# Performance work log

Measured on AMD Instinct MI355X. Metric: run time of the kernel, lower is better.

Reference implementation:

```python
import jax, jax.numpy as jnp
import numpy as np
import math

# ---- hyperparameters (init_kwargs) ----
D = 2              # spatial dimension
MTOT = 65          # quadrature nodes per dimension (odd)
LENGTHSCALE = 0.1  # SE kernel lengthscale
OUTPUTSCALE = 1.0  # SE kernel variance
SIGMASQ = 0.05     # observation noise variance
CG_ITERS = 30      # fixed CG iteration count (replaces tol-based early stopping)
N_TRAIN = 100000
N_TEST = 50000
TWO_PI = 2.0 * math.pi


def setup_inputs() -> dict:
    key = jax.random.key(0)
    k1, k2, k3 = jax.random.split(key, 3)
    x = jax.random.uniform(k1, (N_TRAIN, D), dtype=jnp.float32)
    y = jax.random.normal(k2, (N_TRAIN,), dtype=jnp.float32)
    x_new = jax.random.uniform(k3, (N_TEST, D), dtype=jnp.float32)
    return {"x": x, "y": y, "x_new": x_new}


def _phases(col, h, freqs, isign):
    # exp(isign * i * 2*pi*h * x * k), shape [N, K]
    return jnp.exp((1j * isign * TWO_PI) * (h * col[:, None] * freqs[None, :]).astype(jnp.float32))


def _nudft_type1(pts, c, h, freqs):
    # fk[a,b] = sum_n c_n exp(-2*pi*i*h*(k_a x_n0 + k_b x_n1)); separable tensor grid
    E0 = _phases(pts[:, 0], h, freqs, -1.0)
    E1 = _phases(pts[:, 1], h, freqs, -1.0)
    return jnp.einsum('n,na,nb->ab', c.astype(jnp.complex64), E0, E1)


def _nudft_type2(pts, fk, h, freqs):
    # f_n = sum_{a,b} fk[a,b] exp(+2*pi*i*h*(k_a x_n0 + k_b x_n1))
    E0 = _phases(pts[:, 0], h, freqs, +1.0)
    E1 = _phases(pts[:, 1], h, freqs, +1.0)
    return jnp.einsum('ab,na,nb->n', fk, E0, E1)


def _cg(A, b, iters):
    # complex Hermitian-PSD conjugate gradients, fixed iteration count
    x0 = jnp.zeros_like(b)
    r0 = b
    rs0 = jnp.real(jnp.vdot(r0, r0))

    def step(carry, _):
        xk, r, p, rs = carry
        Ap = A(p)
        alpha = rs / jnp.real(jnp.vdot(p, Ap))
        xk = xk + alpha * p
        r = r - alpha * Ap
        rs_new = jnp.real(jnp.vdot(r, r))
        p = r + (rs_new / rs) * p
        return (xk, r, p, rs_new), None

    (xk, _, _, _), _ = jax.lax.scan(step, (x0, r0, r0, rs0), None, length=iters)
    return xk


def _forward(x, y, x_new):
    m = (MTOT - 1) // 2
    # geometry / quadrature (get_xis): domain extent L, spacing h = 1/L, grid k = -m..m
    x_all = jnp.concatenate((x, x_new), axis=0)
    L = jnp.max(jnp.max(x_all, axis=0) - jnp.min(x_all, axis=0))
    L = jnp.where(L <= 1e-9, jnp.float32(1.0), L)
    h = (1.0 / L).astype(jnp.float32)
    k = (jnp.arange(MTOT) - m).astype(jnp.float32)
    xis_1d = h * k
    X0, X1 = jnp.meshgrid(xis_1d, xis_1d, indexing='ij')
    sq = X0 * X0 + X1 * X1  # [MTOT, MTOT] squared frequency norm
    # squared-exponential spectral density S(s) = sigma_f^2 (2*pi*l^2)^(d/2) exp(-2*pi^2*l^2 |s|^2)
    l2 = LENGTHSCALE * LENGTHSCALE
    spec = OUTPUTSCALE * (TWO_PI * l2) ** (D / 2) * jnp.exp((-2.0 * math.pi ** 2 * l2) * sq)
    ws = jnp.sqrt(spec * h ** D).reshape(-1).astype(jnp.complex64)  # [M]

    # rhs = ws * F^H y  (type-1 NUFFT, exact NUDFT)
    rhs = ws * _nudft_type1(x, y, h, k).reshape(-1)

    # Toeplitz convolution vector v[o] = sum_n exp(-2*pi*i*h*o.x_n), offsets -(mtot-1)..(mtot-1)
    kk = (jnp.arange(2 * MTOT - 1) - (MTOT - 1)).astype(jnp.float32)
    Ev0 = _phases(x[:, 0], h, kk, -1.0)
    Ev1 = _phases(x[:, 1], h, kk, -1.0)
    v = jnp.einsum('na,nb->ab', Ev0, Ev1)  # [2M-1, 2M-1]
    # circularly align offset 0 to index 0, precompute FFT
    v_circ = jnp.roll(v, shift=(-(MTOT - 1), -(MTOT - 1)), axis=(0, 1))
    vhat = jnp.fft.fftn(v_circ)
    s_fft = (2 * MTOT - 1, 2 * MTOT - 1)

    def toeplitz_apply(w):  # w: [MTOT, MTOT] complex
        W = jnp.fft.fftn(w, s=s_fft)
        full = jnp.fft.ifftn(vhat * W)
        return full[:MTOT, :MTOT]

    def A_mean(beta):  # (W F^H F W + sigma^2 I) beta, beta flat [M]
        wb = (ws * beta).reshape(MTOT, MTOT)
        Tw = toeplitz_apply(wb).reshape(-1)
        return ws * Tw + SIGMASQ * beta

    beta = _cg(A_mean, rhs, CG_ITERS)
    # posterior mean at test points via type-2 NUFFT
    yhat = jnp.real(_nudft_type2(x_new, (ws * beta).reshape(MTOT, MTOT), h, k))
    return yhat


def reference(x, y, x_new):
    return _forward(x, y, x_new)
```

## Files before the change

kernel.cpp:

```cpp
#include <hip/hip_runtime.h>
#include <math.h>

#define M2 4225
#define NTRAIN 100000
#define NTEST 50000
#define CGITERS 30
#define TWO_PI_D 6.283185307179586476925287
#define TPI32 6.28318530717958647692f

#define F_H 0
#define F_RS 1
#define F_PAP 2
#define F_RSN 3
#define F_WS 8
#define F_RHS 4234
#define F_X 12684
#define F_R 21134
#define F_P 29584
#define F_AP 38034
#define F_PB 46484
#define F_VF 50710
#define F_VHAT 83992
#define F_PROD 117274
#define D_VPART 125330
#define D_FKPART 2271890

#define NCHUNK 128
#define PTSB2 782
#define VHALF 8385
#define VH2 16770
#define FKHALF 2145
#define FH2 4290

__device__ __forceinline__ unsigned fkey(float f){
  unsigned u = __float_as_uint(f);
  return (u & 0x80000000u) ? ~u : (u | 0x80000000u);
}
__device__ __forceinline__ float fdec(unsigned k){
  unsigned u = (k & 0x80000000u) ? (k & 0x7fffffffu) : ~k;
  return __uint_as_float(u);
}

__global__ void k_init(unsigned* mm){
  if (threadIdx.x == 0){
    mm[0] = 0xFFFFFFFFu; mm[1] = 0u; mm[2] = 0xFFFFFFFFu; mm[3] = 0u;
  }
}

__global__ void k_minmax(const float* __restrict__ x, const float* __restrict__ xn,
                         unsigned* __restrict__ mm){
  int tid = blockIdx.x * blockDim.x + threadIdx.x;
  int str = gridDim.x * blockDim.x;
  float mn0 = 1e30f, mx0 = -1e30f, mn1 = 1e30f, mx1 = -1e30f;
  const float2* a = (const float2*)x;
  for (int i = tid; i < NTRAIN; i += str){
    float2 v = a[i];
    mn0 = fminf(mn0, v.x); mx0 = fmaxf(mx0, v.x);
    mn1 = fminf(mn1, v.y); mx1 = fmaxf(mx1, v.y);
  }
  const float2* b = (const float2*)xn;
  for (int i = tid; i < NTEST; i += str){
    float2 v = b[i];
    mn0 = fminf(mn0, v.x); mx0 = fmaxf(mx0, v.x);
    mn1 = fminf(mn1, v.y); mx1 = fmaxf(mx1, v.y);
  }
  for (int off = 32; off; off >>= 1){
    mn0 = fminf(mn0, __shfl_xor(mn0, off, 64));
    mx0 = fmaxf(mx0, __shfl_xor(mx0, off, 64));
    mn1 = fminf(mn1, __shfl_xor(mn1, off, 64));
    mx1 = fmaxf(mx1, __shfl_xor(mx1, off, 64));
  }
  if ((threadIdx.x & 63) == 0){
    atomicMin(&mm[0], fkey(mn0)); atomicMax(&mm[1], fkey(mx0));
    atomicMin(&mm[2], fkey(mn1)); atomicMax(&mm[3], fkey(mx1));
  }
}

__global__ void k_setup(float* __restrict__ wsf){
  const unsigned* mm = (const unsigned*)(wsf + 4);
  float mn0 = fdec(mm[0]), mx0 = fdec(mm[1]);
  float mn1 = fdec(mm[2]), mx1 = fdec(mm[3]);
  float d0 = __fsub_rn(mx0, mn0), d1 = __fsub_rn(mx1, mn1);
  float L = fmaxf(d0, d1);
  if (L <= 1e-9f) L = 1.0f;
  float hf = __fdiv_rn(1.0f, L);
  if (threadIdx.x == 0) wsf[F_H] = hf;
  const float c0f = (float)(TWO_PI_D * 0.01);
  const float c1f = (float)(-2.0 * 9.869604401089358618834 * 0.01);
  float h2f = __fmul_rn(hf, hf);
  for (int e = threadIdx.x; e < M2; e += blockDim.x){
    int r = e / 65, c = e - r * 65;
    float xi0 = __fmul_rn(hf, (float)(r - 32));
    float xi1 = __fmul_rn(hf, (float)(c - 32));
    float sq = __fadd_rn(__fmul_rn(xi0, xi0), __fmul_rn(xi1, xi1));
    float spec = __fmul_rn(c0f, expf(__fmul_rn(c1f, sq)));
    wsf[F_WS + e] = sqrtf(__fmul_rn(spec, h2f));
  }
}

__launch_bounds__(256)
__global__ void k_vfk(const float* __restrict__ x, const float* __restrict__ y,
                      const float* __restrict__ wsf,
                      double* __restrict__ vpart, double* __restrict__ fkpart){
  __shared__ double2 aL[16][80];
  __shared__ double2 bL[16][32];
  __shared__ float hxs[16][2];
  __shared__ float ys[16];
  const float hf = wsf[F_H];
  const int tid = threadIdx.x;
  const int t0 = tid >> 4, t1 = tid & 15;
  const bool isV = (blockIdx.y < 5);
  const int colbase = (isV ? blockIdx.y : (blockIdx.y - 5)) * 32;
  const int p0 = blockIdx.x * PTSB2;
  const int pend = min(p0 + PTSB2, NTRAIN);

  if (isV){
    double2 acc[5][2];
    #pragma unroll
    for (int k = 0; k < 5; ++k){ acc[k][0] = make_double2(0.0, 0.0); acc[k][1] = make_double2(0.0, 0.0); }
    for (int base = p0; base < pend; base += 16){
      if (tid < 32){
        int p = tid >> 1, d = tid & 1;
        int gp = base + p;
        hxs[p][d] = (gp < pend) ? __fmul_rn(hf, x[2 * gp + d]) : 0.f;
      }
      __syncthreads();
      for (int i = tid; i < 16 * 80; i += 256){
        int p = i / 80;
        int o = i - p * 80;
        int gp = base + p;
        double2 va = make_double2(0.0, 0.0);
        if (gp < pend && o < 65){
          float t = __fmul_rn(hxs[p][0], (float)o);
          float sn, cs; sincosf(__fmul_rn(TPI32, t), &sn, &cs);
          va = make_double2((double)cs, (double)(-sn));
        }
        aL[p][o] = va;
      }
      for (int i = tid; i < 16 * 32; i += 256){
        int p = i >> 5, c = i & 31;
        int gp = base + p;
        int j = colbase + c;
        double2 vb = make_double2(0.0, 0.0);
        if (gp < pend && j < 129){
          float t = __fmul_rn(hxs[p][1], (float)(j - 64));
          float sn, cs; sincosf(__fmul_rn(TPI32, t), &sn, &cs);
          vb = make_double2((double)cs, (double)(-sn));
        }
        bL[p][c] = vb;
      }
      __syncthreads();
      #pragma unroll 1
      for (int p = 0; p < 16; ++p){
        double2 bv0 = bL[p][t1];
        double2 bv1 = bL[p][t1 + 16];
        double2 av[5];
        #pragma unroll
        for (int k = 0; k < 5; ++k) av[k] = aL[p][t0 + 16 * k];
        #pragma unroll
        for (int k = 0; k < 5; ++k){
          acc[k][0].x += av[k].x * bv0.x - av[k].y * bv0.y;
          acc[k][0].y += av[k].x * bv0.y + av[k].y * bv0.x;
          acc[k][1].x += av[k].x * bv1.x - av[k].y * bv1.y;
          acc[k][1].y += av[k].x * bv1.y + av[k].y * bv1.x;
        }
      }
      __syncthreads();
    }
    double* outp = vpart + (size_t)blockIdx.x * VH2;
    #pragma unroll
    for (int k = 0; k < 5; ++k){
      int o0 = t0 + 16 * k;
      if (o0 < 65){
        #pragma unroll
        for (int cc = 0; cc < 2; ++cc){
          int jcol = colbase + t1 + 16 * cc;
          if (jcol < 129){
            int e = o0 * 129 + jcol;
            outp[2 * e] = acc[k][cc].x;
            outp[2 * e + 1] = acc[k][cc].y;
          }
        }
      }
    }
  } else {
    double2 acc[3][2];
    #pragma unroll
    for (int k = 0; k < 3; ++k){ acc[k][0] = make_double2(0.0, 0.0); acc[k][1] = make_double2(0.0, 0.0); }
    for (int base = p0; base < pend; base += 16){
      if (tid < 32){
        int p = tid >> 1, d = tid & 1;
        int gp = base + p;
        hxs[p][d] = (gp < pend) ? __fmul_rn(hf, x[2 * gp + d]) : 0.f;
      } else if (tid < 48){
        int p = tid - 32;
        int gp = base + p;
        ys[p] = (gp < pend) ? y[gp] : 0.f;
      }
      __syncthreads();
      for (int i = tid; i < 16 * 48; i += 256){
        int p = i / 48, o = i - p * 48;
        int gp = base + p;
        double2 val = make_double2(0.0, 0.0);
        if (o < 33 && gp < pend){
          float t = __fmul_rn(hxs[p][0], (float)o);
          float sn, cs; sincosf(__fmul_rn(TPI32, t), &sn, &cs);
          val = make_double2((double)__fmul_rn(ys[p], cs), (double)__fmul_rn(ys[p], -sn));
        }
        aL[p][o] = val;
      }
      for (int i = tid; i < 16 * 32; i += 256){
        int p = i >> 5, c = i & 31;
        int gp = base + p;
        int j = colbase + c;
        double2 vb = make_double2(0.0, 0.0);
        if (gp < pend && j < 65){
          float t = __fmul_rn(hxs[p][1], (float)(j - 32));
          float sn, cs; sincosf(__fmul_rn(TPI32, t), &sn, &cs);
          vb = make_double2((double)cs, (double)(-sn));
        }
        bL[p][c] = vb;
      }
      __syncthreads();
      #pragma unroll 1
      for (int p = 0; p < 16; ++p){
        double2 bv0 = bL[p][t1];
        double2 bv1 = bL[p][t1 + 16];
        double2 av[3];
        #pragma unroll
        for (int k = 0; k < 3; ++k) av[k] = aL[p][t0 + 16 * k];
        #pragma unroll
        for (int k = 0; k < 3; ++k){
          acc[k][0].x += av[k].x * bv0.x - av[k].y * bv0.y;
          acc[k][0].y += av[k].x * bv0.y + av[k].y * bv0.x;
          acc[k][1].x += av[k].x * bv1.x - av[k].y * bv1.y;
          acc[k][1].y += av[k].x * bv1.y + av[k].y * bv1.x;
        }
      }
      __syncthreads();
    }
    double* outp = fkpart + (size_t)blockIdx.x * FH2;
    #pragma unroll
    for (int k = 0; k < 3; ++k){
      int o0 = t0 + 16 * k;
      if (o0 < 33){
        #pragma unroll
        for (int cc = 0; cc < 2; ++cc){
          int jcol = colbase + t1 + 16 * cc;
          if (jcol < 65){
            int e = o0 * 65 + jcol;
            outp[2 * e] = acc[k][cc].x;
            outp[2 * e + 1] = acc[k][cc].y;
          }
        }
      }
    }
  }
}

__global__ void k_reduce_v(const double* __restrict__ wsd, float* __restrict__ wsf){
  int e = blockIdx.x * blockDim.x + threadIdx.x;
  if (e >= VHALF) return;
  const double* vp = wsd + D_VPART;
  double sr = 0.0, si = 0.0;
  for (int k = 0; k < NCHUNK; ++k){
    sr += vp[(size_t)k * VH2 + 2 * e];
    si += vp[(size_t)k * VH2 + 2 * e + 1];
  }
  float r32 = (float)sr, i32 = (float)si;
  int o0 = e / 129, j = e - o0 * 129;
  float2* vF = (float2*)(wsf + F_VF);
  vF[(o0 + 64) * 129 + j] = make_float2(r32, i32);
  if (o0 > 0) vF[(64 - o0) * 129 + (128 - j)] = make_float2(r32, -i32);
}

__global__ void k_reduce_fk(const double* __restrict__ wsd, float* __restrict__ wsf){
  int e = blockIdx.x * blockDim.x + threadIdx.x;
  if (e >= FKHALF) return;
  const double* fp = wsd + D_FKPART;
  double sr = 0.0, si = 0.0;
  for (int k = 0; k < NCHUNK; ++k){
    sr += fp[(size_t)k * FH2 + 2 * e];
    si += fp[(size_t)k * FH2 + 2 * e + 1];
  }
  float fr = (float)sr, fi = (float)si;
  int a = e / 65, c = e - a * 65;
  int ef = (a + 32) * 65 + c;
  float wf = wsf[F_WS + ef];
  float* rhs = wsf + F_RHS;
  rhs[2 * ef] = __fmul_rn(wf, fr);
  rhs[2 * ef + 1] = __fmul_rn(wf, fi);
  if (a > 0){
    int ef2 = (32 - a) * 65 + (64 - c);
    float wf2 = wsf[F_WS + ef2];
    rhs[2 * ef2] = __fmul_rn(wf2, fr);
    rhs[2 * ef2 + 1] = -__fmul_rn(wf2, fi);
  }
}

__launch_bounds__(192)
__global__ void k_vhat(float* __restrict__ wsf){
  __shared__ double twc[129], tws[129];
  __shared__ double t1r[129], t1i[129];
  int p = blockIdx.x, t = threadIdx.x;
  if (t < 129){
    double ang = TWO_PI_D * (double)t / 129.0;
    double s, c; sincos(ang, &s, &c);
    twc[t] = c; tws[t] = s;
  }
  __syncthreads();
  if (t < 129){
    const float2* vF = (const float2*)(wsf + F_VF);
    int n = t;
    int nsrc = (n + 64) % 129;
    double ar = 0.0, ai = 0.0;
    for (int m = 0; m < 129; ++m){
      float2 v = vF[((m + 64) % 129) * 129 + nsrc];
      int idx = (p * m) % 129;
      double wr = twc[idx], wi = -tws[idx];
      ar += (double)v.x * wr - (double)v.y * wi;
      ai += (double)v.x * wi + (double)v.y * wr;
    }
    t1r[n] = ar; t1i[n] = ai;
  }
  __syncthreads();
  if (t < 129){
    int q = t;
    double ar = 0.0, ai = 0.0;
    for (int n = 0; n < 129; ++n){
      int idx = (q * n) % 129;
      double wr = twc[idx], wi = -tws[idx];
      ar += t1r[n] * wr - t1i[n] * wi;
      ai += t1r[n] * wi + t1i[n] * wr;
    }
    ((float2*)(wsf + F_VHAT))[p * 129 + q] = make_float2((float)ar, (float)ai);
  }
}

__global__ void k_cg_init(float* __restrict__ wsf){
  int e = blockIdx.x * blockDim.x + threadIdx.x;
  if (e >= M2) return;
  const float2* rhs = (const float2*)(wsf + F_RHS);
  float2 b = rhs[e];
  ((float2*)(wsf + F_X))[e] = make_float2(0.f, 0.f);
  ((float2*)(wsf + F_R))[e] = b;
  ((float2*)(wsf + F_P))[e] = b;
  wsf[F_PB + e] = __fadd_rn(__fmul_rn(b.x, b.x), __fmul_rn(b.y, b.y));
}

__device__ __forceinline__ float pw_leaf(const float* d, int o, int n){
  float r0 = d[o], r1 = d[o+1], r2 = d[o+2], r3 = d[o+3];
  float r4 = d[o+4], r5 = d[o+5], r6 = d[o+6], r7 = d[o+7];
  int i = 8;
  int lim = n - (n & 7);
  for (; i < lim; i += 8){
    r0 = __fadd_rn(r0, d[o+i]);   r1 = __fadd_rn(r1, d[o+i+1]);
    r2 = __fadd_rn(r2, d[o+i+2]); r3 = __fadd_rn(r3, d[o+i+3]);
    r4 = __fadd_rn(r4, d[o+i+4]); r5 = __fadd_rn(r5, d[o+i+5]);
    r6 = __fadd_rn(r6, d[o+i+6]); r7 = __fadd_rn(r7, d[o+i+7]);
  }
  float res = __fadd_rn(__fadd_rn(__fadd_rn(r0, r1), __fadd_rn(r2, r3)),
                        __fadd_rn(__fadd_rn(r4, r5), __fadd_rn(r6, r7)));
  for (; i < n; ++i) res = __fadd_rn(res, d[o+i]);
  return res;
}

__device__ __forceinline__ void pw_tree(const float* pb, float* T, int tid){
  if (tid < 16){
    const int tb[16] = {0,264,528,792,1056,1320,1584,1848,
                        2112,2376,2640,2904,3168,3432,3696,3960};
    int base = tb[tid];
    int sz3 = (tid == 15) ? 73 : 72;
    float L0 = pw_leaf(pb, base, 128);
    float L1 = pw_leaf(pb, base + 128, 64);
    float L2 = pw_leaf(pb, base + 192, sz3);
    T[tid] = __fadd_rn(L0, __fadd_rn(L1, L2));
  }
  __syncthreads();
  if (tid == 0){
    float s0 = __fadd_rn(__fadd_rn(T[0], T[1]), __fadd_rn(T[2], T[3]));
    float s1 = __fadd_rn(__fadd_rn(T[4], T[5]), __fadd_rn(T[6], T[7]));
    float s2 = __fadd_rn(__fadd_rn(T[8], T[9]), __fadd_rn(T[10], T[11]));
    float s3 = __fadd_rn(__fadd_rn(T[12], T[13]), __fadd_rn(T[14], T[15]));
    T[0] = __fadd_rn(__fadd_rn(s0, s1), __fadd_rn(s2, s3));
  }
}

__launch_bounds__(256)
__global__ void k_pair0(float* __restrict__ wsf){
  __shared__ float pb[M2];
  __shared__ float T[16];
  int tid = threadIdx.x;
  for (int i = tid; i < M2; i += 256) pb[i] = wsf[F_PB + i];
  __syncthreads();
  pw_tree(pb, T, tid);
  __syncthreads();
  if (tid == 0) wsf[F_RS] = T[0];
}

__launch_bounds__(192)
__global__ void k_wfft(float* __restrict__ wsf){
  __shared__ double twc[129], tws[129];
  __shared__ double t1r[65], t1i[65];
  int pr = blockIdx.x, t = threadIdx.x;
  if (t < 129){
    double ang = TWO_PI_D * (double)t / 129.0;
    double s, c; sincos(ang, &s, &c);
    twc[t] = c; tws[t] = s;
  }
  __syncthreads();
  if (t < 65){
    const float2* P = (const float2*)(wsf + F_P);
    const float* W = wsf + F_WS;
    int n = t;
    double ar = 0.0, ai = 0.0;
    for (int m = 0; m < 65; ++m){
      int e = m * 65 + n;
      float2 p = P[e];
      float w = W[e];
      float wbr = __fmul_rn(w, p.x), wbi = __fmul_rn(w, p.y);
      int idx = (pr * m) % 129;
      double wr = twc[idx], wi = -tws[idx];
      ar += (double)wbr * wr - (double)wbi * wi;
      ai += (double)wbr * wi + (double)wbi * wr;
    }
    t1r[n] = ar; t1i[n] = ai;
  }
  __syncthreads();
  if (t < 129){
    int q = t;
    double ar = 0.0, ai = 0.0;
    for (int n = 0; n < 65; ++n){
      int idx = (q * n) % 129;
      double wr = twc[idx], wi = -tws[idx];
      ar += t1r[n] * wr - t1i[n] * wi;
      ai += t1r[n] * wi + t1i[n] * wr;
    }
    float Wr = (float)ar, Wi = (float)ai;
    float2 v = ((const float2*)(wsf + F_VHAT))[pr * 129 + q];
    float prre = __fsub_rn(__fmul_rn(v.x, Wr), __fmul_rn(v.y, Wi));
    float prim = __fadd_rn(__fmul_rn(v.x, Wi), __fmul_rn(v.y, Wr));
    ((float2*)(wsf + F_PROD))[pr * 129 + q] = make_float2(prre, prim);
  }
}

__launch_bounds__(192)
__global__ void k_ifft(float* __restrict__ wsf){
  __shared__ double twc[129], tws[129];
  __shared__ double ur[129], ui[129];
  int m = blockIdx.x, t = threadIdx.x;
  if (t < 129){
    double ang = TWO_PI_D * (double)t / 129.0;
    double s, c; sincos(ang, &s, &c);
    twc[t] = c; tws[t] = s;
  }
  __syncthreads();
  if (t < 129){
    const float2* prod = (const float2*)(wsf + F_PROD);
    int q = t;
    double ar = 0.0, ai = 0.0;
    for (int pr = 0; pr < 129; ++pr){
      float2 v = prod[pr * 129 + q];
      int idx = (m * pr) % 129;
      double wr = twc[idx], wi = tws[idx];
      ar += (double)v.x * wr - (double)v.y * wi;
      ai += (double)v.x * wi + (double)v.y * wr;
    }
    const double sc = 1.0 / 129.0;
    ur[q] = ar * sc; ui[q] = ai * sc;
  }
  __syncthreads();
  if (t < 65){
    int n = t;
    double ar = 0.0, ai = 0.0;
    for (int q = 0; q < 129; ++q){
      int idx = (n * q) % 129;
      double wr = twc[idx], wi = tws[idx];
      ar += ur[q] * wr - ui[q] * wi;
      ai += ur[q] * wi + ui[q] * wr;
    }
    const double sc = 1.0 / 129.0;
    float Twr = (float)(ar * sc), Twi = (float)(ai * sc);
    int e = m * 65 + n;
    float w = wsf[F_WS + e];
    float2 p = ((const float2*)(wsf + F_P))[e];
    float Apx = __fadd_rn(__fmul_rn(w, Twr), __fmul_rn(0.05f, p.x));
    float Apy = __fadd_rn(__fmul_rn(w, Twi), __fmul_rn(0.05f, p.y));
    ((float2*)(wsf + F_AP))[e] = make_float2(Apx, Apy);
    wsf[F_PB + e] = __fadd_rn(__fmul_rn(p.x, Apx), __fmul_rn(p.y, Apy));
  }
}

__launch_bounds__(256)
__global__ void k_cgstep(float* __restrict__ wsf){
  __shared__ float pb[M2];
  __shared__ float T[16];
  __shared__ float sh[2];
  int tid = threadIdx.x;
  for (int i = tid; i < M2; i += 256) pb[i] = wsf[F_PB + i];
  __syncthreads();
  pw_tree(pb, T, tid);
  __syncthreads();
  if (tid == 0){
    float rs = wsf[F_RS];
    sh[1] = rs;
    sh[0] = __fdiv_rn(rs, T[0]);
  }
  __syncthreads();
  float alpha = sh[0];
  float2* X = (float2*)(wsf + F_X);
  float2* R = (float2*)(wsf + F_R);
  float2* P = (float2*)(wsf + F_P);
  const float2* AP = (const float2*)(wsf + F_AP);
  for (int e = tid; e < M2; e += 256){
    float2 p = P[e], ap = AP[e], xv = X[e], rv = R[e];
    xv.x = __fadd_rn(xv.x, __fmul_rn(alpha, p.x));
    xv.y = __fadd_rn(xv.y, __fmul_rn(alpha, p.y));
    rv.x = __fsub_rn(rv.x, __fmul_rn(alpha, ap.x));
    rv.y = __fsub_rn(rv.y, __fmul_rn(alpha, ap.y));
    X[e] = xv; R[e] = rv;
    pb[e] = __fadd_rn(__fmul_rn(rv.x, rv.x), __fmul_rn(rv.y, rv.y));
  }
  __syncthreads();
  pw_tree(pb, T, tid);
  __syncthreads();
  if (tid == 0){
    float rsn = T[0];
    sh[0] = __fdiv_rn(rsn, sh[1]);
    wsf[F_RS] = rsn;
  }
  __syncthreads();
  float beta = sh[0];
  for (int e = tid; e < M2; e += 256){
    float2 rv = R[e], p = P[e];
    P[e] = make_float2(__fadd_rn(rv.x, __fmul_rn(beta, p.x)),
                       __fadd_rn(rv.y, __fmul_rn(beta, p.y)));
  }
}

__launch_bounds__(256)
__global__ void k_predict(const float* __restrict__ xn, const float* __restrict__ wsf,
                          float* __restrict__ out){
  __shared__ double fbRe[M2];
  __shared__ double fbIm[M2];
  const float hf = wsf[F_H];
  const float* wsq = wsf + F_WS;
  const float2* xb = (const float2*)(wsf + F_X);
  int tid = threadIdx.x;
  for (int i = tid; i < M2; i += 256){
    float w = wsq[i]; float2 q = xb[i];
    fbRe[i] = (double)__fmul_rn(w, q.x);
    fbIm[i] = (double)__fmul_rn(w, q.y);
  }
  __syncthreads();
  int lane = tid & 63;
  int wid = (blockIdx.x * 256 + tid) >> 6;
  int nw = (gridDim.x * 256) >> 6;
  for (int n = wid; n < NTEST; n += nw){
    float hx0 = __fmul_rn(hf, xn[2 * n]);
    float hx1 = __fmul_rn(hf, xn[2 * n + 1]);
    float t0 = __fmul_rn(hx0, (float)(lane - 32));
    float s0, c0; sincosf(__fmul_rn(TPI32, t0), &s0, &c0);
    float t1 = __fmul_rn(hx1, (float)(lane - 32));
    float s1, c1; sincosf(__fmul_rn(TPI32, t1), &s1, &c1);
    float t0x = __fmul_rn(hx0, 32.0f);
    float s0x, c0x; sincosf(__fmul_rn(TPI32, t0x), &s0x, &c0x);
    float t1x = __fmul_rn(hx1, 32.0f);
    float s1x, c1x; sincosf(__fmul_rn(TPI32, t1x), &s1x, &c1x);
    double e0r = (double)c0, e0i = (double)s0;
    double e1r = (double)c1, e1i = (double)s1;
    double gr = 0.0, gi = 0.0;
    for (int a = 0; a < 64; ++a){
      double er = __shfl(e0r, a, 64);
      double ei = __shfl(e0i, a, 64);
      double fr = fbRe[a * 65 + lane];
      double fi = fbIm[a * 65 + lane];
      gr += fr * er - fi * ei;
      gi += fr * ei + fi * er;
    }
    {
      double fr = fbRe[64 * 65 + lane], fi = fbIm[64 * 65 + lane];
      gr += fr * (double)c0x - fi * (double)s0x;
      gi += fr * (double)s0x + fi * (double)c0x;
    }
    double contrib = gr * e1r - gi * e1i;
    {
      double fr = fbRe[lane * 65 + 64], fi = fbIm[lane * 65 + 64];
      double ur = fr * e0r - fi * e0i;
      double ui = fr * e0i + fi * e0r;
      contrib += ur * (double)c1x - ui * (double)s1x;
      if (lane == 0){
        double fr2 = fbRe[64 * 65 + 64], fi2 = fbIm[64 * 65 + 64];
        double vr = fr2 * (double)c0x - fi2 * (double)s0x;
        double vi = fr2 * (double)s0x + fi2 * (double)c0x;
        contrib += vr * (double)c1x - vi * (double)s1x;
      }
    }
    for (int off = 32; off; off >>= 1) contrib += __shfl_xor(contrib, off, 64);
    if (lane == 0) out[n] = (float)contrib;
  }
}

extern "C" void kernel_launch(void* const* d_in, const int* in_sizes, int n_in,
                              void* d_out, int out_size, void* d_ws, size_t ws_size,
                              hipStream_t stream){
  const float* x = (const float*)d_in[0];
  const float* y = (const float*)d_in[1];
  const float* xnew = (const float*)d_in[2];
  float* wsf = (float*)d_ws;
  double* wsd = (double*)d_ws;
  float* out = (float*)d_out;
  unsigned* mm = (unsigned*)(wsf + 4);

  k_init<<<1, 64, 0, stream>>>(mm);
  k_minmax<<<256, 256, 0, stream>>>(x, xnew, mm);
  k_setup<<<1, 256, 0, stream>>>(wsf);
  k_vfk<<<dim3(NCHUNK, 8), 256, 0, stream>>>(x, y, wsf, wsd + D_VPART, wsd + D_FKPART);
  k_reduce_v<<<33, 256, 0, stream>>>(wsd, wsf);
  k_reduce_fk<<<9, 256, 0, stream>>>(wsd, wsf);
  k_vhat<<<129, 192, 0, stream>>>(wsf);
  k_cg_init<<<17, 256, 0, stream>>>(wsf);
  k_pair0<<<1, 256, 0, stream>>>(wsf);
  for (int it = 0; it < CGITERS; ++it){
    k_wfft<<<129, 192, 0, stream>>>(wsf);
    k_ifft<<<65, 192, 0, stream>>>(wsf);
    k_cgstep<<<1, 256, 0, stream>>>(wsf);
  }
  k_predict<<<256, 256, 0, stream>>>(xnew, wsf, out);
}
```

Before: 2.173 ms.

## Fuse CG iteration loop into one persistent kernel with grid barriers

Replaces the 90 per-iteration launches (forward DFT, inverse DFT, CG update) with a single persistent kernel of 129 blocks that synchronises through a two-level atomic grid barrier kept in workspace memory. It also replaces the modulo twiddle index computation with an incremental add-and-wrap. The aim is to remove kernel launch and drain overhead across the 30 iterations. In exchange, all 129 blocks must be co-resident for the barrier to avoid deadlock, and blocks sit idle during the single-block CG update phase.

```diff
diff --git a/kernel.cpp b/kernel.cpp
--- a/kernel.cpp
+++ b/kernel.cpp
@@ -22,6 +22,7 @@
 #define F_VF 50710
 #define F_VHAT 83992
 #define F_PROD 117274
+#define U_BAR 150592
 #define D_VPART 125330
 #define D_FKPART 2271890
 
@@ -31,6 +32,7 @@
 #define VH2 16770
 #define FKHALF 2145
 #define FH2 4290
+#define NBLK 129
 
 __device__ __forceinline__ unsigned fkey(float f){
   unsigned u = __float_as_uint(f);
@@ -339,6 +341,7 @@
 
 __global__ void k_cg_init(float* __restrict__ wsf){
   int e = blockIdx.x * blockDim.x + threadIdx.x;
+  if (e < 320) ((unsigned*)wsf)[U_BAR + e] = 0u;
   if (e >= M2) return;
   const float2* rhs = (const float2*)(wsf + F_RHS);
   float2 b = rhs[e];
@@ -398,143 +401,176 @@
   if (tid == 0) wsf[F_RS] = T[0];
 }
 
-__launch_bounds__(192)
-__global__ void k_wfft(float* __restrict__ wsf){
+__device__ __forceinline__ void gridbar(unsigned* bar){
+  __syncthreads();
+  if (threadIdx.x == 0){
+    unsigned* cnt = bar + (blockIdx.x >> 3) * 16;
+    unsigned* top = bar + 272;
+    unsigned* gen = bar + 288;
+    int gsize = ((blockIdx.x >> 3) < 16) ? 8 : 1;
+    __threadfence();
+    unsigned g = __hip_atomic_load(gen, __ATOMIC_RELAXED, __HIP_MEMORY_SCOPE_AGENT);
+    unsigned old = __hip_atomic_fetch_add(cnt, 1u, __ATOMIC_RELAXED, __HIP_MEMORY_SCOPE_AGENT);
+    if ((int)old == gsize - 1){
+      __hip_atomic_store(cnt, 0u, __ATOMIC_RELAXED, __HIP_MEMORY_SCOPE_AGENT);
+      unsigned oldt = __hip_atomic_fetch_add(top, 1u, __ATOMIC_ACQ_REL, __HIP_MEMORY_SCOPE_AGENT);
+      if (oldt == 16u){
+        __hip_atomic_store(top, 0u, __ATOMIC_RELAXED, __HIP_MEMORY_SCOPE_AGENT);
+        __hip_atomic_fetch_add(gen, 1u, __ATOMIC_RELEASE, __HIP_MEMORY_SCOPE_AGENT);
+      } else {
+        while (__hip_atomic_load(gen, __ATOMIC_RELAXED, __HIP_MEMORY_SCOPE_AGENT) == g){
+          __builtin_amdgcn_s_sleep(2);
+        }
+      }
+    } else {
+      while (__hip_atomic_load(gen, __ATOMIC_RELAXED, __HIP_MEMORY_SCOPE_AGENT) == g){
+        __builtin_amdgcn_s_sleep(2);
+      }
+    }
+    __threadfence();
+  }
+  __syncthreads();
+}
+
+__launch_bounds__(256)
+__global__ void k_cgloop(float* __restrict__ wsf){
   __shared__ double twc[129], tws[129];
-  __shared__ double t1r[65], t1i[65];
-  int pr = blockIdx.x, t = threadIdx.x;
+  __shared__ double d1[129], d2[129];
+  __shared__ float pb[M2];
+  __shared__ float T[16];
+  __shared__ float sh[2];
+  const int bid = blockIdx.x;
+  const int t = threadIdx.x;
+  unsigned* bar = ((unsigned*)wsf) + U_BAR;
   if (t < 129){
     double ang = TWO_PI_D * (double)t / 129.0;
     double s, c; sincos(ang, &s, &c);
     twc[t] = c; tws[t] = s;
   }
   __syncthreads();
-  if (t < 65){
-    const float2* P = (const float2*)(wsf + F_P);
-    const float* W = wsf + F_WS;
-    int n = t;
-    double ar = 0.0, ai = 0.0;
-    for (int m = 0; m < 65; ++m){
-      int e = m * 65 + n;
-      float2 p = P[e];
-      float w = W[e];
-      float wbr = __fmul_rn(w, p.x), wbi = __fmul_rn(w, p.y);
-      int idx = (pr * m) % 129;
-      double wr = twc[idx], wi = -tws[idx];
-      ar += (double)wbr * wr - (double)wbi * wi;
-      ai += (double)wbr * wi + (double)wbi * wr;
-    }
-    t1r[n] = ar; t1i[n] = ai;
-  }
-  __syncthreads();
-  if (t < 129){
-    int q = t;
-    double ar = 0.0, ai = 0.0;
-    for (int n = 0; n < 65; ++n){
-      int idx = (q * n) % 129;
-      double wr = twc[idx], wi = -tws[idx];
-      ar += t1r[n] * wr - t1i[n] * wi;
-      ai += t1r[n] * wi + t1i[n] * wr;
-    }
-    float Wr = (float)ar, Wi = (float)ai;
-    float2 v = ((const float2*)(wsf + F_VHAT))[pr * 129 + q];
-    float prre = __fsub_rn(__fmul_rn(v.x, Wr), __fmul_rn(v.y, Wi));
-    float prim = __fadd_rn(__fmul_rn(v.x, Wi), __fmul_rn(v.y, Wr));
-    ((float2*)(wsf + F_PROD))[pr * 129 + q] = make_float2(prre, prim);
-  }
-}
-
-__launch_bounds__(192)
-__global__ void k_ifft(float* __restrict__ wsf){
-  __shared__ double twc[129], tws[129];
-  __shared__ double ur[129], ui[129];
-  int m = blockIdx.x, t = threadIdx.x;
-  if (t < 129){
-    double ang = TWO_PI_D * (double)t / 129.0;
-    double s, c; sincos(ang, &s, &c);
-    twc[t] = c; tws[t] = s;
-  }
-  __syncthreads();
-  if (t < 129){
-    const float2* prod = (const float2*)(wsf + F_PROD);
-    int q = t;
-    double ar = 0.0, ai = 0.0;
-    for (int pr = 0; pr < 129; ++pr){
-      float2 v = prod[pr * 129 + q];
-      int idx = (m * pr) % 129;
-      double wr = twc[idx], wi = tws[idx];
-      ar += (double)v.x * wr - (double)v.y * wi;
-      ai += (double)v.x * wi + (double)v.y * wr;
-    }
-    const double sc = 1.0 / 129.0;
-    ur[q] = ar * sc; ui[q] = ai * sc;
-  }
-  __syncthreads();
-  if (t < 65){
-    int n = t;
-    double ar = 0.0, ai = 0.0;
-    for (int q = 0; q < 129; ++q){
-      int idx = (n * q) % 129;
-      double wr = twc[idx], wi = tws[idx];
-      ar += ur[q] * wr - ui[q] * wi;
-      ai += ur[q] * wi + ui[q] * wr;
-    }
-    const double sc = 1.0 / 129.0;
-    float Twr = (float)(ar * sc), Twi = (float)(ai * sc);
-    int e = m * 65 + n;
-    float w = wsf[F_WS + e];
-    float2 p = ((const float2*)(wsf + F_P))[e];
-    float Apx = __fadd_rn(__fmul_rn(w, Twr), __fmul_rn(0.05f, p.x));
-    float Apy = __fadd_rn(__fmul_rn(w, Twi), __fmul_rn(0.05f, p.y));
-    ((float2*)(wsf + F_AP))[e] = make_float2(Apx, Apy);
-    wsf[F_PB + e] = __fadd_rn(__fmul_rn(p.x, Apx), __fmul_rn(p.y, Apy));
-  }
-}
-
-__launch_bounds__(256)
-__global__ void k_cgstep(float* __restrict__ wsf){
-  __shared__ float pb[M2];
-  __shared__ float T[16];
-  __shared__ float sh[2];
-  int tid = threadIdx.x;
-  for (int i = tid; i < M2; i += 256) pb[i] = wsf[F_PB + i];
-  __syncthreads();
-  pw_tree(pb, T, tid);
-  __syncthreads();
-  if (tid == 0){
-    float rs = wsf[F_RS];
-    sh[1] = rs;
-    sh[0] = __fdiv_rn(rs, T[0]);
-  }
-  __syncthreads();
-  float alpha = sh[0];
+  float2* PROD = (float2*)(wsf + F_PROD);
+  const float2* VHAT = (const float2*)(wsf + F_VHAT);
   float2* X = (float2*)(wsf + F_X);
   float2* R = (float2*)(wsf + F_R);
   float2* P = (float2*)(wsf + F_P);
-  const float2* AP = (const float2*)(wsf + F_AP);
-  for (int e = tid; e < M2; e += 256){
-    float2 p = P[e], ap = AP[e], xv = X[e], rv = R[e];
-    xv.x = __fadd_rn(xv.x, __fmul_rn(alpha, p.x));
-    xv.y = __fadd_rn(xv.y, __fmul_rn(alpha, p.y));
-    rv.x = __fsub_rn(rv.x, __fmul_rn(alpha, ap.x));
-    rv.y = __fsub_rn(rv.y, __fmul_rn(alpha, ap.y));
-    X[e] = xv; R[e] = rv;
-    pb[e] = __fadd_rn(__fmul_rn(rv.x, rv.x), __fmul_rn(rv.y, rv.y));
-  }
-  __syncthreads();
-  pw_tree(pb, T, tid);
-  __syncthreads();
-  if (tid == 0){
-    float rsn = T[0];
-    sh[0] = __fdiv_rn(rsn, sh[1]);
-    wsf[F_RS] = rsn;
-  }
-  __syncthreads();
-  float beta = sh[0];
-  for (int e = tid; e < M2; e += 256){
-    float2 rv = R[e], p = P[e];
-    P[e] = make_float2(__fadd_rn(rv.x, __fmul_rn(beta, p.x)),
-                       __fadd_rn(rv.y, __fmul_rn(beta, p.y)));
+  float2* AP = (float2*)(wsf + F_AP);
+  const float* W = wsf + F_WS;
+
+  for (int it = 0; it < CGITERS; ++it){
+    {
+      const int pr = bid;
+      if (t < 65){
+        int n = t;
+        double ar = 0.0, ai = 0.0;
+        int idx = 0;
+        for (int m = 0; m < 65; ++m){
+          int e = m * 65 + n;
+          float2 p = P[e];
+          float w = W[e];
+          float wbr = __fmul_rn(w, p.x), wbi = __fmul_rn(w, p.y);
+          double wr = twc[idx], wi = -tws[idx];
+          ar += (double)wbr * wr - (double)wbi * wi;
+          ai += (double)wbr * wi + (double)wbi * wr;
+          idx += pr; if (idx >= 129) idx -= 129;
+        }
+        d1[n] = ar; d2[n] = ai;
+      }
+      __syncthreads();
+      if (t < 129){
+        int q = t;
+        double ar = 0.0, ai = 0.0;
+        int idx = 0;
+        for (int n = 0; n < 65; ++n){
+          double wr = twc[idx], wi = -tws[idx];
+          ar += d1[n] * wr - d2[n] * wi;
+          ai += d1[n] * wi + d2[n] * wr;
+          idx += q; if (idx >= 129) idx -= 129;
+        }
+        float Wr = (float)ar, Wi = (float)ai;
+        float2 v = VHAT[pr * 129 + q];
+        float prre = __fsub_rn(__fmul_rn(v.x, Wr), __fmul_rn(v.y, Wi));
+        float prim = __fadd_rn(__fmul_rn(v.x, Wi), __fmul_rn(v.y, Wr));
+        PROD[pr * 129 + q] = make_float2(prre, prim);
+      }
+    }
+    gridbar(bar);
+    if (bid < 65){
+      const int m = bid;
+      if (t < 129){
+        int q = t;
+        double ar = 0.0, ai = 0.0;
+        int idx = 0;
+        for (int pr = 0; pr < 129; ++pr){
+          float2 v = PROD[pr * 129 + q];
+          double wr = twc[idx], wi = tws[idx];
+          ar += (double)v.x * wr - (double)v.y * wi;
+          ai += (double)v.x * wi + (double)v.y * wr;
+          idx += m; if (idx >= 129) idx -= 129;
+        }
+        const double sc = 1.0 / 129.0;
+        d1[q] = ar * sc; d2[q] = ai * sc;
+      }
+      __syncthreads();
+      if (t < 65){
+        int n = t;
+        double ar = 0.0, ai = 0.0;
+        int idx = 0;
+        for (int q = 0; q < 129; ++q){
+          double wr = twc[idx], wi = tws[idx];
+          ar += d1[q] * wr - d2[q] * wi;
+          ai += d1[q] * wi + d2[q] * wr;
+          idx += n; if (idx >= 129) idx -= 129;
+        }
+        const double sc = 1.0 / 129.0;
+        float Twr = (float)(ar * sc), Twi = (float)(ai * sc);
+        int e = m * 65 + n;
+        float w = W[e];
+        float2 p = P[e];
+        float Apx = __fadd_rn(__fmul_rn(w, Twr), __fmul_rn(0.05f, p.x));
+        float Apy = __fadd_rn(__fmul_rn(w, Twi), __fmul_rn(0.05f, p.y));
+        AP[e] = make_float2(Apx, Apy);
+        wsf[F_PB + e] = __fadd_rn(__fmul_rn(p.x, Apx), __fmul_rn(p.y, Apy));
+      }
+    }
+    gridbar(bar);
+    if (bid == 0){
+      for (int i = t; i < M2; i += 256) pb[i] = wsf[F_PB + i];
+      __syncthreads();
+      pw_tree(pb, T, t);
+      __syncthreads();
+      if (t == 0){
+        float rs = wsf[F_RS];
+        sh[1] = rs;
+        sh[0] = __fdiv_rn(rs, T[0]);
+      }
+      __syncthreads();
+      float alpha = sh[0];
+      for (int e = t; e < M2; e += 256){
+        float2 p = P[e], ap = AP[e], xv = X[e], rv = R[e];
+        xv.x = __fadd_rn(xv.x, __fmul_rn(alpha, p.x));
+        xv.y = __fadd_rn(xv.y, __fmul_rn(alpha, p.y));
+        rv.x = __fsub_rn(rv.x, __fmul_rn(alpha, ap.x));
+        rv.y = __fsub_rn(rv.y, __fmul_rn(alpha, ap.y));
+        X[e] = xv; R[e] = rv;
+        pb[e] = __fadd_rn(__fmul_rn(rv.x, rv.x), __fmul_rn(rv.y, rv.y));
+      }
+      __syncthreads();
+      pw_tree(pb, T, t);
+      __syncthreads();
+      if (t == 0){
+        float rsn = T[0];
+        sh[0] = __fdiv_rn(rsn, sh[1]);
+        wsf[F_RS] = rsn;
+      }
+      __syncthreads();
+      float beta = sh[0];
+      for (int e = t; e < M2; e += 256){
+        float2 rv = R[e], p = P[e];
+        P[e] = make_float2(__fadd_rn(rv.x, __fmul_rn(beta, p.x)),
+                           __fadd_rn(rv.y, __fmul_rn(beta, p.y)));
+      }
+    }
+    gridbar(bar);
   }
 }
 
@@ -621,10 +657,6 @@
   k_vhat<<<129, 192, 0, stream>>>(wsf);
   k_cg_init<<<17, 256, 0, stream>>>(wsf);
   k_pair0<<<1, 256, 0, stream>>>(wsf);
-  for (int it = 0; it < CGITERS; ++it){
-    k_wfft<<<129, 192, 0, stream>>>(wsf);
-    k_ifft<<<65, 192, 0, stream>>>(wsf);
-    k_cgstep<<<1, 256, 0, stream>>>(wsf);
-  }
+  k_cgloop<<<NBLK, 256, 0, stream>>>(wsf);
   k_predict<<<256, 256, 0, stream>>>(xnew, wsf, out);
 }
```

After: 2.600 ms. 1.2x slower.
